# Kernel tuning notes

Hardware: AMD Instinct MI355X
Metric: run time of the kernel (lower is better)

The kernel has to match this reference:

```python
import jax, jax.numpy as jnp
import numpy as np

B, S, E, H, C = 64, 512, 768, 768, 9
Q_GCE = 0.7
TAU = 0.7
IGNORE = -100


def setup_inputs() -> dict:
    key = jax.random.key(0)
    k_h, k_w1, k_w2, k_lab, k_drop = jax.random.split(key, 5)
    hidden = jax.random.normal(k_h, (B, S, E), dtype=jnp.float32)
    W1 = jax.random.normal(k_w1, (E, H), dtype=jnp.float32) * (1.0 / np.sqrt(E))
    b1 = jnp.zeros((H,), dtype=jnp.float32)
    W2 = jax.random.normal(k_w2, (H, C), dtype=jnp.float32) * (1.0 / np.sqrt(H))
    b2 = jnp.zeros((C,), dtype=jnp.float32)
    labels = jax.random.randint(k_lab, (B, S), 0, C, dtype=jnp.int64 if jax.config.jax_enable_x64 else jnp.int32)
    drop = jax.random.uniform(k_drop, (B, S)) < 0.1
    labels = jnp.where(drop, IGNORE, labels)
    return {"hidden": hidden, "W1": W1, "b1": b1, "W2": W2, "b2": b2,
            "labels": labels, "epoch": 5}


def reference(hidden, W1, b1, W2, b2, labels, epoch):
    # head: Linear -> Tanh -> Linear (dropout is identity at eval)
    h = jnp.tanh(jnp.einsum('bse,eh->bsh', hidden, W1) + b1)
    logit = jnp.einsum('bsh,hc->bsc', h, W2) + b2
    probs = jax.nn.softmax(logit, axis=2)  # [B,S,C]

    mask = labels != IGNORE
    safe_labels = jnp.where(mask, labels, 0)
    # p_i = probs[i, labels[i]] gathered for every token
    p = jnp.take_along_axis(probs, safe_labels[..., None], axis=2)[..., 0]  # [B,S]
    # GCE weight: w=1 for epoch<=2, else 1 if p>tau else 0 (constant wrt grads)
    w = jnp.where(epoch <= 2, 1.0, jnp.where(p > TAU, 1.0, 0.0))
    w = jax.lax.stop_gradient(w) * mask.astype(probs.dtype)
    loss = jnp.sum(w * (1.0 - jnp.power(p, Q_GCE)) / Q_GCE)
    return probs, loss
```

## Files before the change

### kernel.cpp

```cpp
#include <hip/hip_runtime.h>
#include <hip/hip_bf16.h>
#include <stdint.h>

#define E_ 768
#define H_ 768
#define C_ 9
#define M_TOTAL 32768
#define BM_ 64

typedef __attribute__((ext_vector_type(8))) __bf16 bf16x8;
typedef __attribute__((ext_vector_type(4))) float f32x4;
typedef __attribute__((ext_vector_type(4))) int i32x4;

static_assert(sizeof(bf16x8) == 16, "bf16x8 must be 16B");

__device__ __forceinline__ unsigned short f2bf(float f) {
    __hip_bfloat16 h = __float2bfloat16(f);
    return __builtin_bit_cast(unsigned short, h);
}

__global__ void prep_kernel(const float* __restrict__ W1, const float* __restrict__ W2,
                            unsigned short* __restrict__ W1f, unsigned short* __restrict__ W2f,
                            float* __restrict__ loss_out)
{
    int b = blockIdx.x;
    int n = threadIdx.x;
    if (b < 768) {
        int k = b;
        float v = W1[k * H_ + n];
        int ntile = n >> 4;
        int t = k >> 5;
        int lane = (n & 15) + 16 * ((k >> 3) & 3);
        int j = k & 7;
        W1f[((ntile * 24 + t) * 64 + lane) * 8 + j] = f2bf(v);
    } else {
        for (int it = 0; it < 16; ++it) {
            int tid = it * 768 + n;
            int j    = tid & 7;
            int lane = (tid >> 3) & 63;
            int t    = tid >> 9;
            int cls  = lane & 15;
            int k = t * 32 + (lane >> 4) * 8 + j;
            W2f[tid] = (cls < C_) ? f2bf(W2[k * C_ + cls]) : (unsigned short)0;
        }
        if (n == 0) *loss_out = 0.0f;
    }
}

__launch_bounds__(1024, 4)
__global__ void fused_head_kernel(const float* __restrict__ hidden,
                                  const unsigned short* __restrict__ W1f,
                                  const float* __restrict__ b1,
                                  const unsigned short* __restrict__ W2f,
                                  const float* __restrict__ b2,
                                  const int* __restrict__ labels,
                                  const int* __restrict__ epoch_p,
                                  float* __restrict__ probs,
                                  float* __restrict__ loss)
{
    __shared__ unsigned short Ash[24 * 4 * 512];

    const int tid  = threadIdx.x;
    const int w    = tid >> 6;
    const int lane = tid & 63;
    const int tok0 = blockIdx.x * BM_;
    const int c16  = lane & 15;
    const int q    = lane >> 4;

    {
        const f32x4* hsrc = (const f32x4*)(hidden + (size_t)tok0 * E_);
        #pragma unroll
        for (int i = 0; i < 12; ++i) {
            int slot = i * 1024 + tid;
            int tk = slot / 192;
            int fq = slot - tk * 192;
            f32x4 v = __builtin_nontemporal_load(hsrc + (size_t)tk * 192 + fq);
            int k = fq * 4;
            int t = k >> 5, mt = tk >> 4;
            int lnf = (tk & 15) + 16 * ((k >> 3) & 3);
            int j = k & 7;
            ushort4 pk = { f2bf(v[0]), f2bf(v[1]), f2bf(v[2]), f2bf(v[3]) };
            *(ushort4*)(&Ash[((t * 4 + mt) * 64 + lnf) * 8 + j]) = pk;
        }
    }
    __syncthreads();

    const unsigned short* Wp = W1f + (size_t)(w * 3 * 24) * 512 + lane * 8;

    bf16x8 bA[3], bB[3];
    #pragma unroll
    for (int i = 0; i < 3; ++i)
        bA[i] = __builtin_bit_cast(bf16x8, *(const i32x4*)(Wp + (i * 24 + 0) * 512));
    #pragma unroll
    for (int i = 0; i < 3; ++i)
        bB[i] = __builtin_bit_cast(bf16x8, *(const i32x4*)(Wp + (i * 24 + 1) * 512));

    const f32x4 zero4 = {0.0f, 0.0f, 0.0f, 0.0f};
    f32x4 acc[4][3];
    #pragma unroll
    for (int mt = 0; mt < 4; ++mt)
        #pragma unroll
        for (int nt = 0; nt < 3; ++nt) acc[mt][nt] = zero4;

    #pragma unroll
    for (int tt = 0; tt < 12; ++tt) {
        {
            bf16x8 af[4];
            #pragma unroll
            for (int mt = 0; mt < 4; ++mt)
                af[mt] = __builtin_bit_cast(bf16x8,
                    *(const i32x4*)(&Ash[(((2 * tt) * 4 + mt) * 64 + lane) * 8]));
            #pragma unroll
            for (int mt = 0; mt < 4; ++mt)
                #pragma unroll
                for (int nt = 0; nt < 3; ++nt)
                    acc[mt][nt] = __builtin_amdgcn_mfma_f32_16x16x32_bf16(
                        af[mt], bA[nt], acc[mt][nt], 0, 0, 0);
        }
        if (tt < 11) {
            #pragma unroll
            for (int i = 0; i < 3; ++i)
                bA[i] = __builtin_bit_cast(bf16x8,
                    *(const i32x4*)(Wp + (i * 24 + 2 * tt + 2) * 512));
        }
        {
            bf16x8 af[4];
            #pragma unroll
            for (int mt = 0; mt < 4; ++mt)
                af[mt] = __builtin_bit_cast(bf16x8,
                    *(const i32x4*)(&Ash[(((2 * tt + 1) * 4 + mt) * 64 + lane) * 8]));
            #pragma unroll
            for (int mt = 0; mt < 4; ++mt)
                #pragma unroll
                for (int nt = 0; nt < 3; ++nt)
                    acc[mt][nt] = __builtin_amdgcn_mfma_f32_16x16x32_bf16(
                        af[mt], bB[nt], acc[mt][nt], 0, 0, 0);
        }
        if (tt < 11) {
            #pragma unroll
            for (int i = 0; i < 3; ++i)
                bB[i] = __builtin_bit_cast(bf16x8,
                    *(const i32x4*)(Wp + (i * 24 + 2 * tt + 3) * 512));
        }
    }
    __syncthreads();

    unsigned short* Hsh = &Ash[0];
    f32x4 logit = zero4;
    const int myc = w >> 2;
    for (int c = 0; c < 4; ++c) {
        if (myc == c) {
            #pragma unroll
            for (int i = 0; i < 3; ++i) {
                int kloc = (w & 3) * 48 + i * 16 + c16;
                float b1v = b1[w * 48 + i * 16 + c16];
                int t2 = kloc >> 5;
                int q2 = (kloc >> 3) & 3;
                int j  = kloc & 7;
                #pragma unroll
                for (int mt = 0; mt < 4; ++mt) {
                    #pragma unroll
                    for (int r = 0; r < 4; ++r) {
                        float z = acc[mt][i][r] + b1v;
                        float e = exp2f(z * 2.8853900817779268f);
                        float th = 1.0f - 2.0f * __builtin_amdgcn_rcpf(e + 1.0f);
                        int lanep = (q * 4 + r) + 16 * q2;
                        Hsh[((t2 * 4 + mt) * 64 + lanep) * 8 + j] = f2bf(th);
                    }
                }
            }
        }
        __syncthreads();
        if (w < 4) {
            #pragma unroll
            for (int t2 = 0; t2 < 6; ++t2) {
                bf16x8 ha = __builtin_bit_cast(bf16x8, *(const i32x4*)(&Hsh[((t2 * 4 + w) * 64 + lane) * 8]));
                bf16x8 wb = __builtin_bit_cast(bf16x8, *(const i32x4*)(W2f + ((size_t)(c * 6 + t2) * 64 + lane) * 8));
                logit = __builtin_amdgcn_mfma_f32_16x16x32_bf16(ha, wb, logit, 0, 0, 0);
            }
        }
        __syncthreads();
    }

    if (w < 4) {
        const bool valid = (c16 < C_);
        const float b2v = valid ? b2[c16] : 0.0f;
        const int ep = epoch_p[0];
        float lsum = 0.0f;
        #pragma unroll
        for (int r = 0; r < 4; ++r) {
            float l = valid ? (logit[r] + b2v) : -3.0e38f;
            float m = l;
            #pragma unroll
            for (int d = 1; d < 16; d <<= 1)
                m = fmaxf(m, __shfl_xor(m, d, 64));
            float e = valid ? exp2f((l - m) * 1.44269504f) : 0.0f;
            float s = e;
            #pragma unroll
            for (int d = 1; d < 16; d <<= 1)
                s += __shfl_xor(s, d, 64);
            float p = e / s;
            int row = tok0 + w * 16 + q * 4 + r;
            if (valid) probs[(size_t)row * C_ + c16] = p;
            int lab = labels[row];
            if (valid && lab == c16) {
                float wgt = (ep <= 2) ? 1.0f : ((p > 0.7f) ? 1.0f : 0.0f);
                if (wgt > 0.0f)
                    lsum += (1.0f - exp2f(0.7f * log2f(p))) * (1.0f / 0.7f);
            }
        }
        #pragma unroll
        for (int d = 1; d < 64; d <<= 1)
            lsum += __shfl_xor(lsum, d, 64);
        if (lane == 0) atomicAdd(loss, lsum);
    }
}

extern "C" void kernel_launch(void* const* d_in, const int* in_sizes, int n_in,
                              void* d_out, int out_size, void* d_ws, size_t ws_size,
                              hipStream_t stream)
{
    const float* hidden = (const float*)d_in[0];
    const float* W1     = (const float*)d_in[1];
    const float* b1     = (const float*)d_in[2];
    const float* W2     = (const float*)d_in[3];
    const float* b2     = (const float*)d_in[4];
    const int*   labels = (const int*)d_in[5];
    const int*   epoch  = (const int*)d_in[6];

    float* probs = (float*)d_out;
    float* loss  = probs + (size_t)M_TOTAL * C_;

    unsigned short* W1f = (unsigned short*)d_ws;
    unsigned short* W2f = W1f + 48 * 24 * 512;

    prep_kernel<<<769, 768, 0, stream>>>(W1, W2, W1f, W2f, loss);
    fused_head_kernel<<<M_TOTAL / BM_, 1024, 0, stream>>>(hidden, W1f, b1, W2f, b2,
                                                          labels, epoch, probs, loss);
}
```

Before: 221.5 us.

## Double-buffer hidden-tile loads in LDS and write all tanh activations in one pass

The full upfront staging of the 64x768 hidden tile is replaced by a six-chunk double-buffered pipeline. Global loads for chunk c+1 are issued while the MFMAs consume chunk c, and raw s_barrier is used for synchronisation. The four serialized tanh-write and second-GEMM rounds are collapsed into a single write of the whole H tile followed by one 24-step MFMA chain, which removes several barriers. Probs stores become nontemporal. The hidden-load latency now overlaps the first GEMM, at the cost of more barriers in the main loop and stricter timing for the inline-asm synchronisation.

```diff
diff --git a/kernel.cpp b/kernel.cpp
--- a/kernel.cpp
+++ b/kernel.cpp
@@ -67,26 +67,38 @@
     const int c16  = lane & 15;
     const int q    = lane >> 4;
 
-    {
-        const f32x4* hsrc = (const f32x4*)(hidden + (size_t)tok0 * E_);
-        #pragma unroll
-        for (int i = 0; i < 12; ++i) {
-            int slot = i * 1024 + tid;
-            int tk = slot / 192;
-            int fq = slot - tk * 192;
-            f32x4 v = __builtin_nontemporal_load(hsrc + (size_t)tk * 192 + fq);
-            int k = fq * 4;
-            int t = k >> 5, mt = tk >> 4;
-            int lnf = (tk & 15) + 16 * ((k >> 3) & 3);
-            int j = k & 7;
-            ushort4 pk = { f2bf(v[0]), f2bf(v[1]), f2bf(v[2]), f2bf(v[3]) };
-            *(ushort4*)(&Ash[((t * 4 + mt) * 64 + lnf) * 8 + j]) = pk;
-        }
-    }
-    __syncthreads();
+    const f32x4* hsrc = (const f32x4*)(hidden + (size_t)tok0 * E_);
+    const int tkA = tid >> 5;
+    const int fq  = tid & 31;
+    const int t_l = fq >> 3;
+    const int jj  = (fq & 1) * 4;
+    const int q2s = (fq >> 1) & 3;
+
+    f32x4 rg0, rg1;
+    auto issue = [&](int c) {
+        rg0 = __builtin_nontemporal_load(hsrc + (size_t)tkA * 192 + c * 32 + fq);
+        rg1 = __builtin_nontemporal_load(hsrc + (size_t)(tkA + 32) * 192 + c * 32 + fq);
+    };
+    auto stage = [&](int bsel) {
+        unsigned short* bufp = &Ash[bsel * 8192];
+        {
+            int lnf = (tkA & 15) + 16 * q2s;
+            int mt  = tkA >> 4;
+            ushort4 pk = { f2bf(rg0[0]), f2bf(rg0[1]), f2bf(rg0[2]), f2bf(rg0[3]) };
+            *(ushort4*)(&bufp[((t_l * 4 + mt) * 64 + lnf) * 8 + jj]) = pk;
+        }
+        {
+            int tk  = tkA + 32;
+            int lnf = (tk & 15) + 16 * q2s;
+            int mt  = tk >> 4;
+            ushort4 pk = { f2bf(rg1[0]), f2bf(rg1[1]), f2bf(rg1[2]), f2bf(rg1[3]) };
+            *(ushort4*)(&bufp[((t_l * 4 + mt) * 64 + lnf) * 8 + jj]) = pk;
+        }
+    };
+
+    issue(0);
 
     const unsigned short* Wp = W1f + (size_t)(w * 3 * 24) * 512 + lane * 8;
-
     bf16x8 bA[3], bB[3];
     #pragma unroll
     for (int i = 0; i < 3; ++i)
@@ -102,87 +114,90 @@
         #pragma unroll
         for (int nt = 0; nt < 3; ++nt) acc[mt][nt] = zero4;
 
-    #pragma unroll
-    for (int tt = 0; tt < 12; ++tt) {
-        {
-            bf16x8 af[4];
+    stage(0);
+    asm volatile("s_waitcnt lgkmcnt(0)\ns_barrier" ::: "memory");
+
+    #pragma unroll
+    for (int c = 0; c < 6; ++c) {
+        const unsigned short* bufp = &Ash[(c & 1) * 8192];
+        if (c < 5) issue(c + 1);
+        #pragma unroll
+        for (int tl = 0; tl < 2; ++tl) {
+            const int tt = 2 * c + tl;
+            {
+                bf16x8 af[4];
+                #pragma unroll
+                for (int mt = 0; mt < 4; ++mt)
+                    af[mt] = __builtin_bit_cast(bf16x8,
+                        *(const i32x4*)(&bufp[(((2 * tl) * 4 + mt) * 64 + lane) * 8]));
+                #pragma unroll
+                for (int mt = 0; mt < 4; ++mt)
+                    #pragma unroll
+                    for (int nt = 0; nt < 3; ++nt)
+                        acc[mt][nt] = __builtin_amdgcn_mfma_f32_16x16x32_bf16(
+                            af[mt], bA[nt], acc[mt][nt], 0, 0, 0);
+            }
+            if (tt < 11) {
+                #pragma unroll
+                for (int i = 0; i < 3; ++i)
+                    bA[i] = __builtin_bit_cast(bf16x8,
+                        *(const i32x4*)(Wp + (i * 24 + 2 * tt + 2) * 512));
+            }
+            {
+                bf16x8 af[4];
+                #pragma unroll
+                for (int mt = 0; mt < 4; ++mt)
+                    af[mt] = __builtin_bit_cast(bf16x8,
+                        *(const i32x4*)(&bufp[(((2 * tl + 1) * 4 + mt) * 64 + lane) * 8]));
+                #pragma unroll
+                for (int mt = 0; mt < 4; ++mt)
+                    #pragma unroll
+                    for (int nt = 0; nt < 3; ++nt)
+                        acc[mt][nt] = __builtin_amdgcn_mfma_f32_16x16x32_bf16(
+                            af[mt], bB[nt], acc[mt][nt], 0, 0, 0);
+            }
+            if (tt < 11) {
+                #pragma unroll
+                for (int i = 0; i < 3; ++i)
+                    bB[i] = __builtin_bit_cast(bf16x8,
+                        *(const i32x4*)(Wp + (i * 24 + 2 * tt + 3) * 512));
+            }
+        }
+        if (c < 5) stage((c + 1) & 1);
+        asm volatile("s_waitcnt lgkmcnt(0)\ns_barrier" ::: "memory");
+    }
+
+    unsigned short* Hsh = &Ash[0];
+    #pragma unroll
+    for (int i = 0; i < 3; ++i) {
+        int col = w * 48 + i * 16 + c16;
+        float b1v = b1[col];
+        int t2 = col >> 5;
+        int q2 = (col >> 3) & 3;
+        int j  = col & 7;
+        #pragma unroll
+        for (int mt = 0; mt < 4; ++mt) {
             #pragma unroll
-            for (int mt = 0; mt < 4; ++mt)
-                af[mt] = __builtin_bit_cast(bf16x8,
-                    *(const i32x4*)(&Ash[(((2 * tt) * 4 + mt) * 64 + lane) * 8]));
-            #pragma unroll
-            for (int mt = 0; mt < 4; ++mt)
-                #pragma unroll
-                for (int nt = 0; nt < 3; ++nt)
-                    acc[mt][nt] = __builtin_amdgcn_mfma_f32_16x16x32_bf16(
-                        af[mt], bA[nt], acc[mt][nt], 0, 0, 0);
-        }
-        if (tt < 11) {
-            #pragma unroll
-            for (int i = 0; i < 3; ++i)
-                bA[i] = __builtin_bit_cast(bf16x8,
-                    *(const i32x4*)(Wp + (i * 24 + 2 * tt + 2) * 512));
-        }
-        {
-            bf16x8 af[4];
-            #pragma unroll
-            for (int mt = 0; mt < 4; ++mt)
-                af[mt] = __builtin_bit_cast(bf16x8,
-                    *(const i32x4*)(&Ash[(((2 * tt + 1) * 4 + mt) * 64 + lane) * 8]));
-            #pragma unroll
-            for (int mt = 0; mt < 4; ++mt)
-                #pragma unroll
-                for (int nt = 0; nt < 3; ++nt)
-                    acc[mt][nt] = __builtin_amdgcn_mfma_f32_16x16x32_bf16(
-                        af[mt], bB[nt], acc[mt][nt], 0, 0, 0);
-        }
-        if (tt < 11) {
-            #pragma unroll
-            for (int i = 0; i < 3; ++i)
-                bB[i] = __builtin_bit_cast(bf16x8,
-                    *(const i32x4*)(Wp + (i * 24 + 2 * tt + 3) * 512));
-        }
-    }
-    __syncthreads();
-
-    unsigned short* Hsh = &Ash[0];
-    f32x4 logit = zero4;
-    const int myc = w >> 2;
-    for (int c = 0; c < 4; ++c) {
-        if (myc == c) {
-            #pragma unroll
-            for (int i = 0; i < 3; ++i) {
-                int kloc = (w & 3) * 48 + i * 16 + c16;
-                float b1v = b1[w * 48 + i * 16 + c16];
-                int t2 = kloc >> 5;
-                int q2 = (kloc >> 3) & 3;
-                int j  = kloc & 7;
-                #pragma unroll
-                for (int mt = 0; mt < 4; ++mt) {
-                    #pragma unroll
-                    for (int r = 0; r < 4; ++r) {
-                        float z = acc[mt][i][r] + b1v;
-                        float e = exp2f(z * 2.8853900817779268f);
-                        float th = 1.0f - 2.0f * __builtin_amdgcn_rcpf(e + 1.0f);
-                        int lanep = (q * 4 + r) + 16 * q2;
-                        Hsh[((t2 * 4 + mt) * 64 + lanep) * 8 + j] = f2bf(th);
-                    }
-                }
-            }
-        }
-        __syncthreads();
-        if (w < 4) {
-            #pragma unroll
-            for (int t2 = 0; t2 < 6; ++t2) {
-                bf16x8 ha = __builtin_bit_cast(bf16x8, *(const i32x4*)(&Hsh[((t2 * 4 + w) * 64 + lane) * 8]));
-                bf16x8 wb = __builtin_bit_cast(bf16x8, *(const i32x4*)(W2f + ((size_t)(c * 6 + t2) * 64 + lane) * 8));
-                logit = __builtin_amdgcn_mfma_f32_16x16x32_bf16(ha, wb, logit, 0, 0, 0);
-            }
-        }
-        __syncthreads();
-    }
+            for (int r = 0; r < 4; ++r) {
+                float z = acc[mt][i][r] + b1v;
+                float e = exp2f(z * 2.8853900817779268f);
+                float th = 1.0f - 2.0f * __builtin_amdgcn_rcpf(e + 1.0f);
+                int lanep = (q * 4 + r) + 16 * q2;
+                Hsh[((t2 * 4 + mt) * 64 + lanep) * 8 + j] = f2bf(th);
+            }
+        }
+    }
+    asm volatile("s_waitcnt lgkmcnt(0)\ns_barrier" ::: "memory");
 
     if (w < 4) {
+        f32x4 logit = zero4;
+        #pragma unroll
+        for (int t2 = 0; t2 < 24; ++t2) {
+            bf16x8 ha = __builtin_bit_cast(bf16x8, *(const i32x4*)(&Hsh[((t2 * 4 + w) * 64 + lane) * 8]));
+            bf16x8 wb = __builtin_bit_cast(bf16x8, *(const i32x4*)(W2f + ((size_t)t2 * 64 + lane) * 8));
+            logit = __builtin_amdgcn_mfma_f32_16x16x32_bf16(ha, wb, logit, 0, 0, 0);
+        }
+
         const bool valid = (c16 < C_);
         const float b2v = valid ? b2[c16] : 0.0f;
         const int ep = epoch_p[0];
@@ -201,7 +216,7 @@
                 s += __shfl_xor(s, d, 64);
             float p = e / s;
             int row = tok0 + w * 16 + q * 4 + r;
-            if (valid) probs[(size_t)row * C_ + c16] = p;
+            if (valid) __builtin_nontemporal_store(p, &probs[(size_t)row * C_ + c16]);
             int lab = labels[row];
             if (valid && lab == c16) {
                 float wgt = (ep <= 2) ? 1.0f : ((p > 0.7f) ? 1.0f : 0.0f);
```

After: 219.5 us. About the same (-0.9%).
